# Performance work log

Measured on AMD Instinct MI355X. Metric: run time of the kernel, lower is better.

## Reference

```python
import jax, jax.numpy as jnp
import numpy as np

B, S, HID = 2, 1024, 2048
H, DK, DV = 8, 64, 128
TK, TV = H * DK, H * DV
K = 4                      # conv kernel size
GH = TV // 8               # generator hidden (reduction=8)
EPS = 1e-6


def setup_inputs() -> dict:
    key = jax.random.key(0)
    ks = jax.random.split(key, 10)
    sc = 0.02
    return {
        "hidden_states": jax.random.normal(ks[0], (B, S, HID), jnp.float32),
        "W_qkvabz": jax.random.normal(ks[1], (HID, TK + TK + TV + H + H + TV), jnp.float32) * sc,
        "A_log": jax.random.normal(ks[2], (H,), jnp.float32) * 0.5,
        "dt_bias": jax.random.normal(ks[3], (H,), jnp.float32) * 0.5,
        "conv_state": jax.random.normal(ks[4], (B, TV, K - 1), jnp.float32) * 0.1,
        "w1": jax.random.normal(ks[5], (HID, GH), jnp.float32) * sc,
        "w2": jax.random.normal(ks[6], (GH, TV * K), jnp.float32) * sc,
        "b2": jax.random.normal(ks[7], (TV * K,), jnp.float32) * sc,
        "init_state": jnp.zeros((B, H, DK, DV), jnp.float32),
        "o_norm_w": jnp.ones((DV,), jnp.float32),
        "W_o": jax.random.normal(ks[8], (TV, HID), jnp.float32) * sc,
    }


def _silu(x):
    return x * jax.nn.sigmoid(x)


def _l2norm(x):
    return x * jax.lax.rsqrt(jnp.sum(x * x, axis=-1, keepdims=True) + EPS)


def _dynamic_conv(v, hidden_states, conv_state, w1, w2, b2):
    # per-token depthwise conv kernels from a small MLP
    kernels = (_silu(hidden_states @ w1) @ w2 + b2).reshape(B, S, TV, K)
    # left-pad with cached state (conv_state: [B, TV, K-1] -> [B, K-1, TV])
    x_pad = jnp.concatenate([jnp.swapaxes(conv_state, 1, 2), v], axis=1)  # [B, S+K-1, TV]
    windows = jnp.stack([x_pad[:, j:j + S] for j in range(K)], axis=-1)   # [B, S, TV, K]
    return _silu(jnp.sum(windows * kernels, axis=-1))                      # [B, S, TV]


def _gated_delta_rule(q, k, v, g, beta, init_state):
    # q,k: [B,S,H,DK]; v: [B,S,H,DV]; g,beta: [B,S,H]; state: [B,H,DK,DV]
    q = _l2norm(q) * (DK ** -0.5)
    k = _l2norm(k)

    def step(h, inp):
        q_t, k_t, v_t, g_t, b_t = inp  # [B,H,DK],[B,H,DK],[B,H,DV],[B,H],[B,H]
        h = h * jnp.exp(g_t)[..., None, None]
        kv = jnp.einsum('bhk,bhkv->bhv', k_t, h)
        delta = (v_t - kv) * b_t[..., None]
        h = h + jnp.einsum('bhk,bhv->bhkv', k_t, delta)
        o_t = jnp.einsum('bhk,bhkv->bhv', q_t, h)
        return h, o_t

    xs = (jnp.moveaxis(q, 1, 0), jnp.moveaxis(k, 1, 0), jnp.moveaxis(v, 1, 0),
          jnp.moveaxis(g, 1, 0), jnp.moveaxis(beta, 1, 0))
    _, o = jax.lax.scan(step, init_state, xs)  # o: [S,B,H,DV]
    return jnp.moveaxis(o, 0, 1)               # [B,S,H,DV]


def reference(hidden_states, W_qkvabz, A_log, dt_bias, conv_state, w1, w2, b2,
              init_state, o_norm_w, W_o):
    qkvabz = hidden_states @ W_qkvabz
    q, k, v, a, beta, z = jnp.split(
        qkvabz, np.cumsum([TK, TK, TV, H, H])[:5].tolist(), axis=-1)

    q = _silu(q).reshape(B, S, H, DK)
    k = _silu(k).reshape(B, S, H, DK)

    v = _dynamic_conv(v, hidden_states, conv_state, w1, w2, b2)
    v = v.reshape(B, S, H, DV)

    g = -jnp.exp(A_log) * jax.nn.softplus(a + dt_bias)  # [B,S,H]
    beta = jax.nn.sigmoid(beta)                          # [B,S,H]

    o = _gated_delta_rule(q, k, v, g, beta, init_state)  # [B,S,H,DV]

    # gated RMSNorm: gate first, then normalize (fla GatedRMSNorm)
    z = z.reshape(B, S, H, DV)
    o = o * _silu(z)
    o = o * jax.lax.rsqrt(jnp.mean(o * o, axis=-1, keepdims=True) + EPS) * o_norm_w

    return o.reshape(B, S, TV) @ W_o
```

## Files before the change

### kernel.cpp

```cpp
#include <hip/hip_runtime.h>
#include <hip/hip_bf16.h>
#include <math.h>
#include <stdint.h>

#define BATCH 2
#define SEQ 1024
#define HIDDIM 2048
#define NH 8
#define DKD 64
#define DVD 128
#define TKD 512
#define TVD 1024
#define NCOL 3088
#define KSZ 4
#define NCHK 16

typedef __attribute__((ext_vector_type(8))) short bf16x8;
typedef __attribute__((ext_vector_type(4))) float f32x4;

__device__ __forceinline__ float sigm(float x){ return 1.f/(1.f+expf(-x)); }
__device__ __forceinline__ float siluf(float x){ return x/(1.f+expf(-x)); }
__device__ __forceinline__ float b2f(unsigned short u){
  union { unsigned int i; float f; } x; x.i = ((unsigned int)u) << 16; return x.f;
}
__device__ __forceinline__ unsigned short f2bu(float f){
  __hip_bfloat16 h = __float2bfloat16(f);
  return *(unsigned short*)&h;
}

__device__ __forceinline__ void glds16(const __hip_bfloat16* g, void* l) {
  __builtin_amdgcn_global_load_lds((const __attribute__((address_space(1))) void*)g,
                                   (__attribute__((address_space(3))) void*)l, 16, 0, 0);
}

__global__ __launch_bounds__(256) void cast_k(const float* __restrict__ in,
    unsigned short* __restrict__ out, int n4)
{
  int i = blockIdx.x*256 + threadIdx.x;
  if (i >= n4) return;
  float4 v = ((const float4*)in)[i];
  ushort4 o;
  o.x = f2bu(v.x); o.y = f2bu(v.y); o.z = f2bu(v.z); o.w = f2bu(v.w);
  ((ushort4*)out)[i] = o;
}

__global__ __launch_bounds__(256) void tcast_k(const float* __restrict__ in,
    __hip_bfloat16* __restrict__ out, int R, int C, int Cpad)
{
  __shared__ float tile[32][33];
  const int tx = threadIdx.x & 31, ty = threadIdx.x >> 5;
  const int c = blockIdx.x*32 + tx;
  #pragma unroll
  for (int i = 0; i < 4; ++i) {
    int r = blockIdx.y*32 + ty + i*8;
    tile[ty + i*8][tx] = (c < C) ? in[(size_t)r*C + c] : 0.f;
  }
  __syncthreads();
  #pragma unroll
  for (int i = 0; i < 4; ++i) {
    int orow = blockIdx.x*32 + ty + i*8;
    int ocol = blockIdx.y*32 + tx;
    out[(size_t)orow*R + ocol] = __float2bfloat16(tile[tx][ty + i*8]);
  }
}

template<int EPI>
__global__ __launch_bounds__(256) void mgemm_k(
    const __hip_bfloat16* __restrict__ A,
    const __hip_bfloat16* __restrict__ Bt,
    const float* __restrict__ bias,
    float* __restrict__ Cf, __hip_bfloat16* __restrict__ Cb,
    int M, int N, int K, int nbx)
{
  __shared__ __hip_bfloat16 As[64*32];
  __shared__ __hip_bfloat16 Bs[128*32];
  const int tid = threadIdx.x;
  const int w = tid >> 6, l = tid & 63;
  const int wr = w >> 1, wc = w & 1;
  const int nwg = gridDim.x, q = nwg >> 3;
  const int swz = (blockIdx.x & 7)*q + (blockIdx.x >> 3);
  const int bx = swz % nbx, by = swz / nbx;
  const int row0 = by*64, col0 = bx*128;
  const int fr = l & 15, fq = l >> 4;

  f32x4 acc[2][4];
  #pragma unroll
  for (int m = 0; m < 2; ++m)
    #pragma unroll
    for (int n = 0; n < 4; ++n)
      acc[m][n] = (f32x4){0.f,0.f,0.f,0.f};

  const int ra = w*16 + (l >> 2), ca = (l & 3)*8;
  const int e0 = w*512 + l*8;
  const int rb = e0 >> 5, cb = e0 & 31;

  for (int k0 = 0; k0 < K; k0 += 32) {
    glds16(&A[(size_t)(row0 + ra)*K + k0 + ca],       (char*)As + w*1024);
    glds16(&Bt[(size_t)(col0 + rb)*K + k0 + cb],      (char*)Bs + w*1024);
    glds16(&Bt[(size_t)(col0 + rb + 64)*K + k0 + cb], (char*)Bs + 4096 + w*1024);
    __syncthreads();

    bf16x8 af[2], bfv[4];
    #pragma unroll
    for (int m = 0; m < 2; ++m)
      af[m] = *(const bf16x8*)&As[(wr*32 + m*16 + fr)*32 + fq*8];
    #pragma unroll
    for (int n = 0; n < 4; ++n)
      bfv[n] = *(const bf16x8*)&Bs[(wc*64 + n*16 + fr)*32 + fq*8];
    #pragma unroll
    for (int m = 0; m < 2; ++m)
      #pragma unroll
      for (int n = 0; n < 4; ++n)
        acc[m][n] = __builtin_amdgcn_mfma_f32_16x16x32_bf16(af[m], bfv[n], acc[m][n], 0, 0, 0);
    __syncthreads();
  }

  #pragma unroll
  for (int n = 0; n < 4; ++n) {
    const int ccol = col0 + wc*64 + n*16 + fr;
    #pragma unroll
    for (int m = 0; m < 2; ++m) {
      #pragma unroll
      for (int r = 0; r < 4; ++r) {
        const int crow = row0 + wr*32 + m*16 + fq*4 + r;
        float v = acc[m][n][r];
        if (EPI == 0) {
          Cf[(size_t)crow*N + ccol] = v;
        } else if (EPI == 2) {
          Cb[(size_t)crow*N + ccol] = __float2bfloat16(v + bias[ccol]);
        } else {
          if (ccol < NCOL)       Cf[(size_t)crow*NCOL + ccol] = v;
          else if (ccol >= 3200) Cb[(size_t)crow*128 + (ccol - 3200)] = __float2bfloat16(siluf(v));
        }
      }
    }
  }
}

__global__ __launch_bounds__(256) void actv_k(const float* __restrict__ qkvabz,
    const float* __restrict__ A_log, const float* __restrict__ dt_bias,
    float* __restrict__ kn, unsigned short* __restrict__ qnb,
    unsigned short* __restrict__ knb,
    float* __restrict__ g, float* __restrict__ beta)
{
  int gid = blockIdx.x*4 + (threadIdx.x >> 6);
  int lane = threadIdx.x & 63;
  int row = gid >> 3; int h = gid & 7;
  const float* base = qkvabz + (size_t)row * NCOL;
  float qv = base[h*64 + lane];
  float kv = base[TKD + h*64 + lane];
  float sq = siluf(qv), sk = siluf(kv);
  float ssq = sq*sq, ssk = sk*sk;
  #pragma unroll
  for (int o = 32; o; o >>= 1) { ssq += __shfl_xor(ssq, o); ssk += __shfl_xor(ssk, o); }
  float qn_v = sq * rsqrtf(ssq + 1e-6f) * 0.125f;
  float kn_v = sk * rsqrtf(ssk + 1e-6f);
  size_t idx = (size_t)row*TKD + h*64 + lane;
  kn[idx]  = kn_v;
  qnb[idx] = f2bu(qn_v);
  knb[idx] = f2bu(kn_v);
  if (lane == 0) {
    float av = base[2048 + h] + dt_bias[h];
    float sp = fmaxf(av, 0.f) + log1pf(expf(-fabsf(av)));
    g[(size_t)row*NH + h] = -expf(A_log[h]) * sp;
    float bv = base[2056 + h];
    beta[(size_t)row*NH + h] = sigm(bv);
  }
}

__global__ __launch_bounds__(256) void conv_k(const float* __restrict__ qkvabz,
   const __hip_bfloat16* __restrict__ kern, const float* __restrict__ conv_state,
   float* __restrict__ vconv)
{
  int idx = blockIdx.x*256 + threadIdx.x;
  int c = idx & (TVD-1);
  int bs = idx >> 10;
  int s = bs & (SEQ-1); int b = bs >> 10;
  ushort4 kf = *(const ushort4*)&kern[(size_t)idx * 4];
  float kj[4] = { b2f(kf.x), b2f(kf.y), b2f(kf.z), b2f(kf.w) };
  float acc = 0.f;
  #pragma unroll
  for (int j = 0; j < 4; ++j) {
    int i = s + j;
    float xv = (i < 3) ? conv_state[((size_t)b*TVD + c)*3 + i]
                       : qkvabz[((size_t)(b*SEQ + (i-3)))*NCOL + TKD*2 + c];
    acc = fmaf(xv, kj[j], acc);
  }
  vconv[idx] = siluf(acc);
}

__global__ __launch_bounds__(256) void chunkA_k(const float* __restrict__ kn,
   const unsigned short* __restrict__ knb,
   const float* __restrict__ vconv, const float* __restrict__ gb,
   const float* __restrict__ bb, float* __restrict__ Gcbuf,
   float* __restrict__ Dbuf, float* __restrict__ Bvec,
   unsigned short* __restrict__ UvT, unsigned short* __restrict__ WnTb)
{
  const int blk = blockIdx.x;
  const int bh = blk >> 4, c = blk & 15;
  const int b = bh >> 3, h = bh & 7;
  const int tid = threadIdx.x;
  const int w = tid >> 6, l = tid & 63;
  const int fr = l & 15, fq = l >> 4;
  const int row0 = b*SEQ + c*64;

  __shared__ unsigned short Kb[64*72];
  __shared__ float Xv[64][132];
  __shared__ float Xw[64][68];
  __shared__ float AK[64][68];
  __shared__ float Gsh[64], Bsh[64];

  #pragma unroll
  for (int j = 0; j < 2; ++j) {
    int lin = tid + j*256; int t = lin >> 3, dq = (lin & 7)*8;
    *(uint4*)&Kb[t*72+dq] = *(const uint4*)&knb[(size_t)(row0+t)*TKD + h*64 + dq];
  }
  #pragma unroll
  for (int i = 0; i < 8; ++i) {
    int lin = tid + i*256; int t = lin >> 5, v4 = (lin & 31)*4;
    float4 vv = *(const float4*)&vconv[(size_t)(row0+t)*TVD + h*128 + v4];
    Xv[t][v4]=vv.x; Xv[t][v4+1]=vv.y; Xv[t][v4+2]=vv.z; Xv[t][v4+3]=vv.w;
  }
  if (tid < 64) {
    float gv = gb[(size_t)(row0+tid)*NH + h];
    #pragma unroll
    for (int o = 1; o < 64; o <<= 1) {
      float oth = __shfl_up(gv, o);
      if (tid >= o) gv += oth;
    }
    Gsh[tid] = gv;
    Bsh[tid] = bb[(size_t)(row0+tid)*NH + h];
    Gcbuf[(size_t)blk*64 + tid] = gv;
  }
  __syncthreads();

  {
    f32x4 accS[4];
    #pragma unroll
    for (int n = 0; n < 4; ++n) accS[n] = (f32x4){0.f,0.f,0.f,0.f};
    #pragma unroll
    for (int k0 = 0; k0 < 2; ++k0) {
      bf16x8 a = *(const bf16x8*)&Kb[(w*16+fr)*72 + k0*32 + fq*8];
      #pragma unroll
      for (int n = 0; n < 4; ++n) {
        bf16x8 bb2 = *(const bf16x8*)&Kb[(n*16+fr)*72 + k0*32 + fq*8];
        accS[n] = __builtin_amdgcn_mfma_f32_16x16x32_bf16(a, bb2, accS[n], 0, 0, 0);
      }
    }
    #pragma unroll
    for (int n = 0; n < 4; ++n)
      #pragma unroll
      for (int r = 0; r < 4; ++r) {
        int t = w*16 + fq*4 + r, s = n*16 + fr;
        AK[t][s] = (s < t) ? Bsh[t]*expf(Gsh[t]-Gsh[s])*accS[n][r] : 0.f;
      }
  }
  #pragma unroll
  for (int i = 0; i < 4; ++i) {
    int lin = tid + i*256; int t = lin >> 4, d4 = (lin & 15)*4;
    float4 kv = *(const float4*)&kn[(size_t)(row0+t)*TKD + h*64 + d4];
    float f = Bsh[t]*expf(Gsh[t]);
    Xw[t][d4+0]=f*kv.x; Xw[t][d4+1]=f*kv.y; Xw[t][d4+2]=f*kv.z; Xw[t][d4+3]=f*kv.w;
  }
  __syncthreads();

  if (tid < 192) {
    float x[64];
    if (tid < 128) {
      #pragma unroll
      for (int t = 0; t < 64; ++t) x[t] = Bsh[t]*Xv[t][tid];
    } else {
      #pragma unroll
      for (int t = 0; t < 64; ++t) x[t] = Xw[t][tid-128];
    }
    #pragma unroll
    for (int t = 1; t < 64; ++t) {
      float a0=0.f, a1=0.f, a2=0.f, a3=0.f;
      #pragma unroll
      for (int s4 = 0; s4 < (t+3)/4; ++s4) {
        float4 av = *(const float4*)&AK[t][s4*4];
        a0 = fmaf(av.x, x[s4*4+0], a0);
        a1 = fmaf(av.y, x[s4*4+1], a1);
        a2 = fmaf(av.z, x[s4*4+2], a2);
        a3 = fmaf(av.w, x[s4*4+3], a3);
      }
      x[t] -= (a0+a1)+(a2+a3);
    }
    if (tid < 128) {
      #pragma unroll
      for (int t = 0; t < 64; ++t) Xv[t][tid] = x[t];
    } else {
      #pragma unroll
      for (int t = 0; t < 64; ++t) Xw[t][tid-128] = x[t];
    }
  }
  __syncthreads();

  const float Gtot = Gsh[63];
  #pragma unroll
  for (int i = 0; i < 4; ++i) {
    int lin = tid + i*256; int t = lin >> 4, d4 = (lin & 15)*4;
    float4 kv = *(const float4*)&kn[(size_t)(row0+t)*TKD + h*64 + d4];
    float f = expf(Gtot - Gsh[t]);
    AK[t][d4+0]=f*kv.x; AK[t][d4+1]=f*kv.y; AK[t][d4+2]=f*kv.z; AK[t][d4+3]=f*kv.w;
  }
  __syncthreads();

  {
    const int d1b = (tid >> 4)*4, d2b = (tid & 15)*4;
    float dacc[4][4] = {};
    #pragma unroll 8
    for (int t = 0; t < 64; ++t) {
      float4 kw = *(const float4*)&AK[t][d1b];
      float4 wv = *(const float4*)&Xw[t][d2b];
      float kwa[4] = {kw.x,kw.y,kw.z,kw.w};
      float wva[4] = {wv.x,wv.y,wv.z,wv.w};
      #pragma unroll
      for (int i = 0; i < 4; ++i)
        #pragma unroll
        for (int j = 0; j < 4; ++j)
          dacc[i][j] = fmaf(kwa[i], wva[j], dacc[i][j]);
    }
    const float eG = expf(Gtot);
    #pragma unroll
    for (int i = 0; i < 4; ++i) {
      float vals[4];
      #pragma unroll
      for (int j = 0; j < 4; ++j) {
        float v = -dacc[i][j];
        if (d1b + i == d2b + j) v += eG;
        vals[j] = v;
      }
      *(float4*)&Dbuf[(size_t)blk*4096 + (d1b+i)*64 + d2b] =
        make_float4(vals[0],vals[1],vals[2],vals[3]);
    }
  }
  {
    const int d1b = (tid >> 4)*4, vb = (tid & 15)*8;
    float bacc[4][8] = {};
    #pragma unroll 4
    for (int t = 0; t < 64; ++t) {
      float4 kw = *(const float4*)&AK[t][d1b];
      float4 u0 = *(const float4*)&Xv[t][vb];
      float4 u1 = *(const float4*)&Xv[t][vb+4];
      float kwa[4] = {kw.x,kw.y,kw.z,kw.w};
      float ua[8] = {u0.x,u0.y,u0.z,u0.w,u1.x,u1.y,u1.z,u1.w};
      #pragma unroll
      for (int i = 0; i < 4; ++i)
        #pragma unroll
        for (int j = 0; j < 8; ++j)
          bacc[i][j] = fmaf(kwa[i], ua[j], bacc[i][j]);
    }
    #pragma unroll
    for (int i = 0; i < 4; ++i) {
      *(float4*)&Bvec[(size_t)blk*8192 + (d1b+i)*128 + vb] =
        make_float4(bacc[i][0],bacc[i][1],bacc[i][2],bacc[i][3]);
      *(float4*)&Bvec[(size_t)blk*8192 + (d1b+i)*128 + vb + 4] =
        make_float4(bacc[i][4],bacc[i][5],bacc[i][6],bacc[i][7]);
    }
  }

  {
    #pragma unroll
    for (int i = 0; i < 32; ++i) {
      int v = w*32 + i;
      UvT[(size_t)blk*8192 + v*64 + l] = f2bu(Xv[l][v]);
    }
    #pragma unroll
    for (int i = 0; i < 16; ++i) {
      int d = w*16 + i;
      WnTb[(size_t)blk*4096 + d*64 + l] = f2bu(-Xw[l][d]);
    }
  }
}

__global__ __launch_bounds__(256) void chunkB2_k(const float* __restrict__ Dbuf,
   const float* __restrict__ Bvec, const float* __restrict__ init,
   unsigned short* __restrict__ HcT)
{
  const int blk = blockIdx.x;
  const int bh = blk >> 3, grp = blk & 7;
  const int v0 = grp*16;
  const int tid = threadIdx.x;
  const int v = tid & 15;
  const int d1b = (tid >> 4) * 4;
  __shared__ float DT[64][68];
  __shared__ float bsh[64][17];
  __shared__ float hsh[64][17];

  float hreg[4];
  #pragma unroll
  for (int j = 0; j < 4; ++j) {
    hreg[j] = init[((size_t)bh*64 + d1b + j)*128 + v0 + v];
    hsh[d1b + j][v] = hreg[j];
  }
  float Dreg[16], breg[4];
  {
    const float* Dp = Dbuf + (size_t)(bh*16)*4096;
    const float* bp = Bvec + (size_t)(bh*16)*8192;
    #pragma unroll
    for (int i = 0; i < 16; ++i) Dreg[i] = Dp[tid + i*256];
    #pragma unroll
    for (int i = 0; i < 4; ++i)  breg[i] = bp[(size_t)((tid>>4) + i*16)*128 + v0 + v];
  }
  #pragma unroll
  for (int i = 0; i < 16; ++i) {
    int cell = tid + i*256; DT[cell & 63][cell >> 6] = Dreg[i];
  }
  #pragma unroll
  for (int i = 0; i < 4; ++i) bsh[(tid>>4) + i*16][v] = breg[i];
  __syncthreads();

  for (int c = 0; c < 16; ++c) {
    if (c < 15) {
      const float* Dn = Dbuf + (size_t)(bh*16 + c + 1)*4096;
      const float* bn = Bvec + (size_t)(bh*16 + c + 1)*8192;
      #pragma unroll
      for (int i = 0; i < 16; ++i) Dreg[i] = Dn[tid + i*256];
      #pragma unroll
      for (int i = 0; i < 4; ++i)  breg[i] = bn[(size_t)((tid>>4) + i*16)*128 + v0 + v];
    }
    #pragma unroll
    for (int j = 0; j < 4; ++j)
      HcT[(size_t)(bh*16 + c)*8192 + (size_t)(v0+v)*64 + d1b + j] = f2bu(hreg[j]);
    float nh[4];
    #pragma unroll
    for (int j = 0; j < 4; ++j) nh[j] = bsh[d1b + j][v];
    #pragma unroll 8
    for (int d2 = 0; d2 < 64; ++d2) {
      float hv = hsh[d2][v];
      float4 dv = *(const float4*)&DT[d2][d1b];
      nh[0] = fmaf(dv.x, hv, nh[0]);
      nh[1] = fmaf(dv.y, hv, nh[1]);
      nh[2] = fmaf(dv.z, hv, nh[2]);
      nh[3] = fmaf(dv.w, hv, nh[3]);
    }
    __syncthreads();
    #pragma unroll
    for (int j = 0; j < 4; ++j) { hreg[j] = nh[j]; hsh[d1b + j][v] = nh[j]; }
    if (c < 15) {
      #pragma unroll
      for (int i = 0; i < 16; ++i) {
        int cell = tid + i*256; DT[cell & 63][cell >> 6] = Dreg[i];
      }
      #pragma unroll
      for (int i = 0; i < 4; ++i) bsh[(tid>>4) + i*16][v] = breg[i];
    }
    __syncthreads();
  }
}

__global__ __launch_bounds__(256) void chunkC_k(
   const unsigned short* __restrict__ qnb, const unsigned short* __restrict__ knb,
   const unsigned short* __restrict__ UvT, const unsigned short* __restrict__ WnTb,
   const float* __restrict__ Gcbuf, const unsigned short* __restrict__ HcT,
   float* __restrict__ oattn)
{
  const int blk = blockIdx.x; const int bh = blk >> 4, c = blk & 15;
  const int b = bh >> 3, h = bh & 7;
  const int row0 = b*SEQ + c*64;
  const int tid = threadIdx.x;
  const int w = tid >> 6, l = tid & 63;
  const int fr = l & 15, fq = l >> 4;

  __shared__ unsigned short Qs[64*72];
  __shared__ unsigned short Ks[64*72];
  __shared__ unsigned short Ws[64*72];
  __shared__ unsigned short hT[128*72];
  __shared__ unsigned short UT[128*72];
  __shared__ unsigned short Ss[64*72];
  __shared__ float Gsh[64], Esh[64];

  #pragma unroll
  for (int j = 0; j < 2; ++j) {
    int lin = tid + j*256; int t = lin >> 3, dq = (lin & 7)*8;
    *(uint4*)&Qs[t*72+dq] = *(const uint4*)&qnb[(size_t)(row0+t)*TKD + h*64 + dq];
    *(uint4*)&Ks[t*72+dq] = *(const uint4*)&knb[(size_t)(row0+t)*TKD + h*64 + dq];
    *(uint4*)&Ws[t*72+dq] = *(const uint4*)&WnTb[(size_t)blk*4096 + t*64 + dq];
  }
  #pragma unroll
  for (int j = 0; j < 4; ++j) {
    int lin = tid + j*256; int v = lin >> 3, dq = (lin & 7)*8;
    *(uint4*)&hT[v*72+dq] = *(const uint4*)&HcT[(size_t)blk*8192 + (size_t)v*64 + dq];
    *(uint4*)&UT[v*72+dq] = *(const uint4*)&UvT[(size_t)blk*8192 + (size_t)v*64 + dq];
  }
  if (tid < 64) { float g = Gcbuf[(size_t)blk*64 + tid]; Gsh[tid] = g; Esh[tid] = expf(g); }
  __syncthreads();

  f32x4 accS[4];
  #pragma unroll
  for (int n = 0; n < 4; ++n) accS[n] = (f32x4){0.f,0.f,0.f,0.f};
  #pragma unroll
  for (int k0 = 0; k0 < 2; ++k0) {
    bf16x8 a = *(const bf16x8*)&Qs[(w*16+fr)*72 + k0*32 + fq*8];
    #pragma unroll
    for (int n = 0; n < 4; ++n) {
      bf16x8 bb = *(const bf16x8*)&Ks[(n*16+fr)*72 + k0*32 + fq*8];
      accS[n] = __builtin_amdgcn_mfma_f32_16x16x32_bf16(a, bb, accS[n], 0, 0, 0);
    }
  }
  #pragma unroll
  for (int n = 0; n < 4; ++n)
    #pragma unroll
    for (int r = 0; r < 4; ++r) {
      int t = w*16 + fq*4 + r, s = n*16 + fr;
      float val = (s <= t) ? expf(Gsh[t]-Gsh[s]) * accS[n][r] : 0.f;
      Ss[t*72 + s] = f2bu(val);
    }

  f32x4 accQ[4];
  #pragma unroll
  for (int n = 0; n < 4; ++n) {
    #pragma unroll
    for (int r = 0; r < 4; ++r) {
      int t = w*16 + fq*4 + r, d = n*16 + fr;
      accQ[n][r] = Esh[t] * b2f(Qs[t*72 + d]);
    }
    #pragma unroll
    for (int k0 = 0; k0 < 2; ++k0) {
      bf16x8 a = *(const bf16x8*)&Ss[(w*16+fr)*72 + k0*32 + fq*8];
      bf16x8 bb = *(const bf16x8*)&Ws[(n*16+fr)*72 + k0*32 + fq*8];
      accQ[n] = __builtin_amdgcn_mfma_f32_16x16x32_bf16(a, bb, accQ[n], 0, 0, 0);
    }
  }
  __syncthreads();

  #pragma unroll
  for (int n = 0; n < 4; ++n)
    #pragma unroll
    for (int r = 0; r < 4; ++r) {
      int t = w*16 + fq*4 + r, d = n*16 + fr;
      Ks[t*72 + d] = f2bu(accQ[n][r]);
    }

  #pragma unroll
  for (int n = 0; n < 8; ++n) {
    f32x4 acc = (f32x4){0.f,0.f,0.f,0.f};
    #pragma unroll
    for (int k0 = 0; k0 < 2; ++k0) {
      bf16x8 a1 = *(const bf16x8*)&Ks[(w*16+fr)*72 + k0*32 + fq*8];
      bf16x8 b1 = *(const bf16x8*)&hT[(n*16+fr)*72 + k0*32 + fq*8];
      acc = __builtin_amdgcn_mfma_f32_16x16x32_bf16(a1, b1, acc, 0, 0, 0);
      bf16x8 a2 = *(const bf16x8*)&Ss[(w*16+fr)*72 + k0*32 + fq*8];
      bf16x8 b2v = *(const bf16x8*)&UT[(n*16+fr)*72 + k0*32 + fq*8];
      acc = __builtin_amdgcn_mfma_f32_16x16x32_bf16(a2, b2v, acc, 0, 0, 0);
    }
    #pragma unroll
    for (int r = 0; r < 4; ++r) {
      int t = w*16 + fq*4 + r, v = n*16 + fr;
      oattn[(size_t)(row0+t)*TVD + h*128 + v] = acc[r];
    }
  }
}

__global__ __launch_bounds__(256) void norm_k(const float* __restrict__ oattn,
   const float* __restrict__ qkvabz, const float* __restrict__ onw,
   __hip_bfloat16* __restrict__ ofin)
{
  int gid = blockIdx.x*4 + (threadIdx.x >> 6);
  int lane = threadIdx.x & 63;
  int row = gid >> 3; int h = gid & 7;
  size_t ob = (size_t)row*TVD + h*128;
  float2 ov = *(const float2*)&oattn[ob + lane*2];
  float2 zv = *(const float2*)&qkvabz[(size_t)row*NCOL + 2064 + h*128 + lane*2];
  float g0 = ov.x * siluf(zv.x), g1 = ov.y * siluf(zv.y);
  float ss = g0*g0 + g1*g1;
  #pragma unroll
  for (int o = 32; o; o >>= 1) ss += __shfl_xor(ss, o);
  float r = rsqrtf(ss * (1.f/128.f) + 1e-6f);
  ofin[ob + lane*2]     = __float2bfloat16(g0 * r * onw[lane*2]);
  ofin[ob + lane*2 + 1] = __float2bfloat16(g1 * r * onw[lane*2+1]);
}

extern "C" void kernel_launch(void* const* d_in, const int* in_sizes, int n_in,
                              void* d_out, int out_size, void* d_ws, size_t ws_size,
                              hipStream_t stream) {
  const float* hidden     = (const float*)d_in[0];
  const float* Wqkvabz    = (const float*)d_in[1];
  const float* A_log      = (const float*)d_in[2];
  const float* dt_bias    = (const float*)d_in[3];
  const float* conv_state = (const float*)d_in[4];
  const float* w1         = (const float*)d_in[5];
  const float* w2         = (const float*)d_in[6];
  const float* b2         = (const float*)d_in[7];
  const float* init_state = (const float*)d_in[8];
  const float* o_norm_w   = (const float*)d_in[9];
  const float* W_o        = (const float*)d_in[10];
  float* out = (float*)d_out;

  float* ws = (float*)d_ws;
  float* qkvabz = ws;
  float* kern   = qkvabz + (size_t)6324224;
  float* qn     = kern   + (size_t)8388608;
  float* kn     = qn     + (size_t)1048576;
  float* gbuf   = kn     + (size_t)1048576;
  float* bbuf   = gbuf   + (size_t)16384;
  float* vconv  = bbuf   + (size_t)16384;
  float* bfpool = vconv  + (size_t)2097152;
  __hip_bfloat16* hidden_bf = (__hip_bfloat16*)bfpool;
  __hip_bfloat16* w1t   = hidden_bf + (size_t)4194304;
  __hip_bfloat16* w2t   = w1t + (size_t)262144;
  __hip_bfloat16* Wot   = w2t + (size_t)524288;
  __hip_bfloat16* x1sb  = Wot + (size_t)2097152;
  __hip_bfloat16* ofinb = x1sb + (size_t)262144;
  float* Gcbuf  = (float*)(ofinb + (size_t)2097152);
  __hip_bfloat16* Wcat   = (__hip_bfloat16*)kern;
  __hip_bfloat16* kernbf = (__hip_bfloat16*)kern;
  float* oattn  = kern;
  float* Dbuf   = kern + (size_t)2097152;
  float* Bvec   = kern + (size_t)3145728;
  unsigned short* UvTb  = (unsigned short*)(kern + (size_t)5242880);
  unsigned short* WnTbb = (unsigned short*)(kern + (size_t)6291456);
  unsigned short* qnb   = (unsigned short*)(kern + (size_t)6815744);
  unsigned short* knb   = (unsigned short*)(kern + (size_t)7340032);
  unsigned short* HcTb  = (unsigned short*)vconv;

  dim3 blk(256);
  cast_k<<<4096, blk, 0, stream>>>(hidden, (unsigned short*)hidden_bf, 1048576);
  tcast_k<<<dim3(100,64), blk, 0, stream>>>(Wqkvabz, Wcat, 2048, 3088, 3200);
  tcast_k<<<dim3(4,64),   blk, 0, stream>>>(w1, Wcat + (size_t)3200*2048, 2048, 128, 128);
  tcast_k<<<dim3(128,4),  blk, 0, stream>>>(w2,  w2t, 128, 4096, 4096);
  tcast_k<<<dim3(64,32),  blk, 0, stream>>>(W_o, Wot, 1024, 2048, 2048);
  mgemm_k<3><<<dim3(832),  blk, 0, stream>>>(hidden_bf, Wcat, nullptr, qkvabz, x1sb, 2048, 3328, 2048, 26);
  mgemm_k<2><<<dim3(1024), blk, 0, stream>>>(x1sb, w2t, b2, nullptr, kernbf, 2048, 4096, 128, 32);
  actv_k<<<4096, blk, 0, stream>>>(qkvabz, A_log, dt_bias, kn, qnb, knb, gbuf, bbuf);
  conv_k<<<8192, blk, 0, stream>>>(qkvabz, kernbf, conv_state, vconv);
  chunkA_k<<<256, blk, 0, stream>>>(kn, knb, vconv, gbuf, bbuf, Gcbuf, Dbuf, Bvec, UvTb, WnTbb);
  chunkB2_k<<<128, blk, 0, stream>>>(Dbuf, Bvec, init_state, HcTb);
  chunkC_k<<<256, blk, 0, stream>>>(qnb, knb, UvTb, WnTbb, Gcbuf, HcTb, oattn);
  norm_k<<<4096, blk, 0, stream>>>(oattn, qkvabz, o_norm_w, ofinb);
  mgemm_k<0><<<dim3(512),  blk, 0, stream>>>(ofinb, Wot, nullptr, out, nullptr, 2048, 2048, 1024, 16);
}
```

Measured before the change: 196.0 us.

## Double-buffer GEMM LDS tiles and merge prep and activation launches

The GEMM now keeps two LDS buffers and issues the next k-tile's global-to-LDS loads before computing on the current one, so memory latency can overlap MFMA work while still using a single barrier per iteration. The five cast and transpose launches are merged into one prep kernel that picks its task by block index. The activation and conv kernels are likewise merged into one launch. This trades extra LDS per block, which may lower occupancy, for less load stall time and fewer kernel launches.

```diff
diff --git a/kernel.cpp b/kernel.cpp
--- a/kernel.cpp
+++ b/kernel.cpp
@@ -33,33 +33,39 @@
                                    (__attribute__((address_space(3))) void*)l, 16, 0, 0);
 }
 
-__global__ __launch_bounds__(256) void cast_k(const float* __restrict__ in,
-    unsigned short* __restrict__ out, int n4)
-{
-  int i = blockIdx.x*256 + threadIdx.x;
-  if (i >= n4) return;
-  float4 v = ((const float4*)in)[i];
-  ushort4 o;
-  o.x = f2bu(v.x); o.y = f2bu(v.y); o.z = f2bu(v.z); o.w = f2bu(v.w);
-  ((ushort4*)out)[i] = o;
-}
-
-__global__ __launch_bounds__(256) void tcast_k(const float* __restrict__ in,
-    __hip_bfloat16* __restrict__ out, int R, int C, int Cpad)
+__global__ __launch_bounds__(256) void prep_k(
+    const float* __restrict__ Wqkvabz, const float* __restrict__ w1,
+    const float* __restrict__ w2, const float* __restrict__ W_o,
+    const float* __restrict__ hidden,
+    __hip_bfloat16* __restrict__ Wcat, __hip_bfloat16* __restrict__ w2t,
+    __hip_bfloat16* __restrict__ Wot, unsigned short* __restrict__ hidden_bf)
 {
   __shared__ float tile[32][33];
+  const int blk = blockIdx.x;
+  const float* in; __hip_bfloat16* out; int R, C, bx, by;
+  if (blk < 6400)      { in=Wqkvabz; out=Wcat; R=2048; C=3088; bx=blk%100; by=blk/100; }
+  else if (blk < 6656) { int t=blk-6400; in=w1;  out=Wcat+(size_t)3200*2048; R=2048; C=128;  bx=t%4;   by=t/4; }
+  else if (blk < 7168) { int t=blk-6656; in=w2;  out=w2t; R=128;  C=4096; bx=t%128; by=t/128; }
+  else if (blk < 9216) { int t=blk-7168; in=W_o; out=Wot; R=1024; C=2048; bx=t%64;  by=t/64; }
+  else {
+    int i = (blk - 9216)*256 + threadIdx.x;
+    float4 v = ((const float4*)hidden)[i];
+    ushort4 o; o.x=f2bu(v.x); o.y=f2bu(v.y); o.z=f2bu(v.z); o.w=f2bu(v.w);
+    ((ushort4*)hidden_bf)[i] = o;
+    return;
+  }
   const int tx = threadIdx.x & 31, ty = threadIdx.x >> 5;
-  const int c = blockIdx.x*32 + tx;
+  const int c = bx*32 + tx;
   #pragma unroll
   for (int i = 0; i < 4; ++i) {
-    int r = blockIdx.y*32 + ty + i*8;
+    int r = by*32 + ty + i*8;
     tile[ty + i*8][tx] = (c < C) ? in[(size_t)r*C + c] : 0.f;
   }
   __syncthreads();
   #pragma unroll
   for (int i = 0; i < 4; ++i) {
-    int orow = blockIdx.x*32 + ty + i*8;
-    int ocol = blockIdx.y*32 + tx;
+    int orow = bx*32 + ty + i*8;
+    int ocol = by*32 + tx;
     out[(size_t)orow*R + ocol] = __float2bfloat16(tile[tx][ty + i*8]);
   }
 }
@@ -72,8 +78,8 @@
     float* __restrict__ Cf, __hip_bfloat16* __restrict__ Cb,
     int M, int N, int K, int nbx)
 {
-  __shared__ __hip_bfloat16 As[64*32];
-  __shared__ __hip_bfloat16 Bs[128*32];
+  __shared__ __hip_bfloat16 As[2][64*32];
+  __shared__ __hip_bfloat16 Bs[2][128*32];
   const int tid = threadIdx.x;
   const int w = tid >> 6, l = tid & 63;
   const int wr = w >> 1, wc = w & 1;
@@ -94,25 +100,36 @@
   const int e0 = w*512 + l*8;
   const int rb = e0 >> 5, cb = e0 & 31;
 
+  const __hip_bfloat16* pA  = &A[(size_t)(row0 + ra)*K + ca];
+  const __hip_bfloat16* pB0 = &Bt[(size_t)(col0 + rb)*K + cb];
+  const __hip_bfloat16* pB1 = &Bt[(size_t)(col0 + rb + 64)*K + cb];
+
+  glds16(pA,  (char*)&As[0][0] + w*1024);
+  glds16(pB0, (char*)&Bs[0][0] + w*1024);
+  glds16(pB1, (char*)&Bs[0][0] + 4096 + w*1024);
+  __syncthreads();
+
+  int cur = 0;
   for (int k0 = 0; k0 < K; k0 += 32) {
-    glds16(&A[(size_t)(row0 + ra)*K + k0 + ca],       (char*)As + w*1024);
-    glds16(&Bt[(size_t)(col0 + rb)*K + k0 + cb],      (char*)Bs + w*1024);
-    glds16(&Bt[(size_t)(col0 + rb + 64)*K + k0 + cb], (char*)Bs + 4096 + w*1024);
-    __syncthreads();
-
+    if (k0 + 32 < K) {
+      glds16(pA  + k0 + 32, (char*)&As[cur^1][0] + w*1024);
+      glds16(pB0 + k0 + 32, (char*)&Bs[cur^1][0] + w*1024);
+      glds16(pB1 + k0 + 32, (char*)&Bs[cur^1][0] + 4096 + w*1024);
+    }
     bf16x8 af[2], bfv[4];
     #pragma unroll
     for (int m = 0; m < 2; ++m)
-      af[m] = *(const bf16x8*)&As[(wr*32 + m*16 + fr)*32 + fq*8];
+      af[m] = *(const bf16x8*)&As[cur][(wr*32 + m*16 + fr)*32 + fq*8];
     #pragma unroll
     for (int n = 0; n < 4; ++n)
-      bfv[n] = *(const bf16x8*)&Bs[(wc*64 + n*16 + fr)*32 + fq*8];
+      bfv[n] = *(const bf16x8*)&Bs[cur][(wc*64 + n*16 + fr)*32 + fq*8];
     #pragma unroll
     for (int m = 0; m < 2; ++m)
       #pragma unroll
       for (int n = 0; n < 4; ++n)
         acc[m][n] = __builtin_amdgcn_mfma_f32_16x16x32_bf16(af[m], bfv[n], acc[m][n], 0, 0, 0);
     __syncthreads();
+    cur ^= 1;
   }
 
   #pragma unroll
@@ -137,56 +154,54 @@
   }
 }
 
-__global__ __launch_bounds__(256) void actv_k(const float* __restrict__ qkvabz,
+__global__ __launch_bounds__(256) void ac_k(const float* __restrict__ qkvabz,
     const float* __restrict__ A_log, const float* __restrict__ dt_bias,
+    const __hip_bfloat16* __restrict__ kern, const float* __restrict__ conv_state,
     float* __restrict__ kn, unsigned short* __restrict__ qnb,
     unsigned short* __restrict__ knb,
-    float* __restrict__ g, float* __restrict__ beta)
+    float* __restrict__ g, float* __restrict__ beta, float* __restrict__ vconv)
 {
-  int gid = blockIdx.x*4 + (threadIdx.x >> 6);
-  int lane = threadIdx.x & 63;
-  int row = gid >> 3; int h = gid & 7;
-  const float* base = qkvabz + (size_t)row * NCOL;
-  float qv = base[h*64 + lane];
-  float kv = base[TKD + h*64 + lane];
-  float sq = siluf(qv), sk = siluf(kv);
-  float ssq = sq*sq, ssk = sk*sk;
-  #pragma unroll
-  for (int o = 32; o; o >>= 1) { ssq += __shfl_xor(ssq, o); ssk += __shfl_xor(ssk, o); }
-  float qn_v = sq * rsqrtf(ssq + 1e-6f) * 0.125f;
-  float kn_v = sk * rsqrtf(ssk + 1e-6f);
-  size_t idx = (size_t)row*TKD + h*64 + lane;
-  kn[idx]  = kn_v;
-  qnb[idx] = f2bu(qn_v);
-  knb[idx] = f2bu(kn_v);
-  if (lane == 0) {
-    float av = base[2048 + h] + dt_bias[h];
-    float sp = fmaxf(av, 0.f) + log1pf(expf(-fabsf(av)));
-    g[(size_t)row*NH + h] = -expf(A_log[h]) * sp;
-    float bv = base[2056 + h];
-    beta[(size_t)row*NH + h] = sigm(bv);
-  }
-}
-
-__global__ __launch_bounds__(256) void conv_k(const float* __restrict__ qkvabz,
-   const __hip_bfloat16* __restrict__ kern, const float* __restrict__ conv_state,
-   float* __restrict__ vconv)
-{
-  int idx = blockIdx.x*256 + threadIdx.x;
-  int c = idx & (TVD-1);
-  int bs = idx >> 10;
-  int s = bs & (SEQ-1); int b = bs >> 10;
-  ushort4 kf = *(const ushort4*)&kern[(size_t)idx * 4];
-  float kj[4] = { b2f(kf.x), b2f(kf.y), b2f(kf.z), b2f(kf.w) };
-  float acc = 0.f;
-  #pragma unroll
-  for (int j = 0; j < 4; ++j) {
-    int i = s + j;
-    float xv = (i < 3) ? conv_state[((size_t)b*TVD + c)*3 + i]
-                       : qkvabz[((size_t)(b*SEQ + (i-3)))*NCOL + TKD*2 + c];
-    acc = fmaf(xv, kj[j], acc);
-  }
-  vconv[idx] = siluf(acc);
+  if (blockIdx.x < 4096) {
+    int gid = blockIdx.x*4 + (threadIdx.x >> 6);
+    int lane = threadIdx.x & 63;
+    int row = gid >> 3; int h = gid & 7;
+    const float* base = qkvabz + (size_t)row * NCOL;
+    float qv = base[h*64 + lane];
+    float kv = base[TKD + h*64 + lane];
+    float sq = siluf(qv), sk = siluf(kv);
+    float ssq = sq*sq, ssk = sk*sk;
+    #pragma unroll
+    for (int o = 32; o; o >>= 1) { ssq += __shfl_xor(ssq, o); ssk += __shfl_xor(ssk, o); }
+    float qn_v = sq * rsqrtf(ssq + 1e-6f) * 0.125f;
+    float kn_v = sk * rsqrtf(ssk + 1e-6f);
+    size_t idx = (size_t)row*TKD + h*64 + lane;
+    kn[idx]  = kn_v;
+    qnb[idx] = f2bu(qn_v);
+    knb[idx] = f2bu(kn_v);
+    if (lane == 0) {
+      float av = base[2048 + h] + dt_bias[h];
+      float sp = fmaxf(av, 0.f) + log1pf(expf(-fabsf(av)));
+      g[(size_t)row*NH + h] = -expf(A_log[h]) * sp;
+      float bv = base[2056 + h];
+      beta[(size_t)row*NH + h] = sigm(bv);
+    }
+  } else {
+    int idx = (blockIdx.x - 4096)*256 + threadIdx.x;
+    int c = idx & (TVD-1);
+    int bs = idx >> 10;
+    int s = bs & (SEQ-1); int b = bs >> 10;
+    ushort4 kf = *(const ushort4*)&kern[(size_t)idx * 4];
+    float kj[4] = { b2f(kf.x), b2f(kf.y), b2f(kf.z), b2f(kf.w) };
+    float acc = 0.f;
+    #pragma unroll
+    for (int j = 0; j < 4; ++j) {
+      int i = s + j;
+      float xv = (i < 3) ? conv_state[((size_t)b*TVD + c)*3 + i]
+                         : qkvabz[((size_t)(b*SEQ + (i-3)))*NCOL + TKD*2 + c];
+      acc = fmaf(xv, kj[j], acc);
+    }
+    vconv[idx] = siluf(acc);
+  }
 }
 
 __global__ __launch_bounds__(256) void chunkA_k(const float* __restrict__ kn,
@@ -616,15 +631,12 @@
   unsigned short* HcTb  = (unsigned short*)vconv;
 
   dim3 blk(256);
-  cast_k<<<4096, blk, 0, stream>>>(hidden, (unsigned short*)hidden_bf, 1048576);
-  tcast_k<<<dim3(100,64), blk, 0, stream>>>(Wqkvabz, Wcat, 2048, 3088, 3200);
-  tcast_k<<<dim3(4,64),   blk, 0, stream>>>(w1, Wcat + (size_t)3200*2048, 2048, 128, 128);
-  tcast_k<<<dim3(128,4),  blk, 0, stream>>>(w2,  w2t, 128, 4096, 4096);
-  tcast_k<<<dim3(64,32),  blk, 0, stream>>>(W_o, Wot, 1024, 2048, 2048);
+  prep_k<<<13312, blk, 0, stream>>>(Wqkvabz, w1, w2, W_o, hidden,
+                                    Wcat, w2t, Wot, (unsigned short*)hidden_bf);
   mgemm_k<3><<<dim3(832),  blk, 0, stream>>>(hidden_bf, Wcat, nullptr, qkvabz, x1sb, 2048, 3328, 2048, 26);
   mgemm_k<2><<<dim3(1024), blk, 0, stream>>>(x1sb, w2t, b2, nullptr, kernbf, 2048, 4096, 128, 32);
-  actv_k<<<4096, blk, 0, stream>>>(qkvabz, A_log, dt_bias, kn, qnb, knb, gbuf, bbuf);
-  conv_k<<<8192, blk, 0, stream>>>(qkvabz, kernbf, conv_state, vconv);
+  ac_k<<<12288, blk, 0, stream>>>(qkvabz, A_log, dt_bias, kernbf, conv_state,
+                                  kn, qnb, knb, gbuf, bbuf, vconv);
   chunkA_k<<<256, blk, 0, stream>>>(kn, knb, vconv, gbuf, bbuf, Gcbuf, Dbuf, Bvec, UvTb, WnTbb);
   chunkB2_k<<<128, blk, 0, stream>>>(Dbuf, Bvec, init_state, HcTb);
   chunkC_k<<<256, blk, 0, stream>>>(qnb, knb, UvTb, WnTbb, Gcbuf, HcTb, oattn);
```

After: 181.7 us. 1.08x faster.
